# Performance work log

Measured on AMD Instinct MI355X. Metric: run time of the kernel, lower is better.

The kernel has to match this reference:

```python
import jax, jax.numpy as jnp
import numpy as np

DIM = 1536
NH = 12
HD = DIM // NH          # 128
C = HD // 2             # 64 complex freq slots per head
DT = C - 2 * (C // 3)   # 22 temporal
DS = C // 3             # 21 per spatial axis
EPS = 1e-6
M_TAB = 64              # rope table length (>= max(f,h,w))


def _rope_tables():
    def tab(d):
        inv = 1.0 / (10000.0 ** (np.arange(d, dtype=np.float64) / d))
        ang = np.outer(np.arange(M_TAB, dtype=np.float64), inv)
        return np.cos(ang), np.sin(ang)
    ct, st = tab(DT)
    ch, sh = tab(DS)
    cw, sw = tab(DS)
    fc = np.concatenate([ct, ch, cw], axis=1).astype(np.float32)  # [M, 64]
    fs = np.concatenate([st, sh, sw], axis=1).astype(np.float32)
    return jnp.asarray(fc), jnp.asarray(fs)


def setup_inputs() -> dict:
    key = jax.random.key(0)
    ks = jax.random.split(key, 6)
    B, F, H, W = 1, 8, 22, 40
    L = F * H * W  # 7040
    s = 0.02
    x = jax.random.normal(ks[0], (B, L, DIM), jnp.float32)
    Wq = jax.random.normal(ks[1], (DIM, DIM), jnp.float32) * s
    Wk = jax.random.normal(ks[2], (DIM, DIM), jnp.float32) * s
    Wv = jax.random.normal(ks[3], (DIM, DIM), jnp.float32) * s
    Wo = jax.random.normal(ks[4], (DIM, DIM), jnp.float32) * s
    bk2 = jax.random.split(ks[5], 4)
    bq = jax.random.normal(bk2[0], (DIM,), jnp.float32) * s
    bk = jax.random.normal(bk2[1], (DIM,), jnp.float32) * s
    bv = jax.random.normal(bk2[2], (DIM,), jnp.float32) * s
    bo = jax.random.normal(bk2[3], (DIM,), jnp.float32) * s
    fc, fs = _rope_tables()
    return dict(x=x, Wq=Wq, bq=bq, Wk=Wk, bk=bk, Wv=Wv, bv=bv, Wo=Wo, bo=bo,
                gq=jnp.ones((DIM,), jnp.float32), gk=jnp.ones((DIM,), jnp.float32),
                freqs_cos=fc, freqs_sin=fs,
                num_frames=F, grid_h=H, grid_w=W,
                chunk_size=2, sink_size=1, max_attention_size=2640)


def _pos_table(tab, f, h, w):
    # tab: [M, 64] -> per-token [f*h*w, 64] via (t,h,w) axis split [22,21,21]
    t = jnp.broadcast_to(tab[:f, :DT][:, None, None, :], (f, h, w, DT))
    hh = jnp.broadcast_to(tab[:h, DT:DT + DS][None, :, None, :], (f, h, w, DS))
    ww = jnp.broadcast_to(tab[:w, DT + DS:][None, None, :, :], (f, h, w, DS))
    return jnp.concatenate([t, hh, ww], axis=-1).reshape(f * h * w, C)


def _forward(x, Wq, bq, Wk, bk, Wv, bv, Wo, bo, gq, gk, freqs_cos, freqs_sin,
             num_frames, grid_h, grid_w, chunk_size, sink_size, max_attention_size):
    B, L, D = x.shape
    lin = lambda t, W, b: jnp.einsum('bld,ed->ble', t, W) + b
    rms = lambda t, g: t * jax.lax.rsqrt(jnp.mean(t * t, axis=-1, keepdims=True) + EPS) * g

    q = rms(lin(x, Wq, bq), gq).reshape(B, L, NH, HD)
    k = rms(lin(x, Wk, bk), gk).reshape(B, L, NH, HD)
    v = lin(x, Wv, bv).reshape(B, L, NH, HD)

    # causal RoPE (start_frame=0)
    cosL = _pos_table(freqs_cos, num_frames, grid_h, grid_w)  # [L, 64]
    sinL = _pos_table(freqs_sin, num_frames, grid_h, grid_w)

    def rope(t):
        a = t.reshape(B, L, NH, C, 2)
        xr, xi = a[..., 0], a[..., 1]
        co = cosL[None, :, None, :]
        si = sinL[None, :, None, :]
        return jnp.stack([xr * co - xi * si, xr * si + xi * co], axis=-1).reshape(B, L, NH, HD)

    q = rope(q)
    k = rope(k)

    # loop attention, diffusion forcing: chunk i attends [0,(i+1)*block) with sink+window
    frame_seqlen = grid_h * grid_w
    block = frame_seqlen * chunk_size
    total_len = num_frames * frame_seqlen
    sink_end = sink_size * frame_seqlen
    num_chunks = -(-total_len // block)
    scale = 1.0 / (HD ** 0.5)

    def attn(qi, ki, vi):
        s = jnp.einsum('bqnd,bknd->bnqk', qi, ki) * scale
        p = jax.nn.softmax(s, axis=-1)
        return jnp.einsum('bnqk,bknd->bqnd', p, vi)

    outs = []
    for i in range(num_chunks):
        q_start = i * block
        q_end = min((i + 1) * block, total_len)
        qi = q[:, q_start:q_end]
        chunk_end = q_end
        if max_attention_size == -1 or sink_end == 0:
            if max_attention_size == -1:
                ki, vi = k[:, :chunk_end], v[:, :chunk_end]
            else:
                ws = max(0, chunk_end - max_attention_size)
                ki, vi = k[:, ws:chunk_end], v[:, ws:chunk_end]
        else:
            window = max_attention_size - sink_end
            ws = max(sink_end, chunk_end - window)
            ki = jnp.concatenate([k[:, :sink_end], k[:, ws:chunk_end]], axis=1)
            vi = jnp.concatenate([v[:, :sink_end], v[:, ws:chunk_end]], axis=1)
        outs.append(attn(qi, ki, vi))

    o = jnp.concatenate(outs, axis=1).reshape(B, L, D)
    return jnp.einsum('bld,ed->ble', o, Wo) + bo


def reference(x, Wq, bq, Wk, bk, Wv, bv, Wo, bo, gq, gk, freqs_cos, freqs_sin,
              num_frames, grid_h, grid_w, chunk_size, sink_size, max_attention_size):
    return _forward(x, Wq, bq, Wk, bk, Wv, bv, Wo, bo, gq, gk, freqs_cos, freqs_sin,
                    num_frames, grid_h, grid_w, chunk_size, sink_size, max_attention_size)
```

## Files before the change

kernel.cpp:

```cpp
#include <hip/hip_runtime.h>
#include <math.h>

typedef __attribute__((ext_vector_type(8))) short short8;
typedef __attribute__((ext_vector_type(4))) float f32x4;
typedef __attribute__((ext_vector_type(16))) float f32x16;
typedef __attribute__((ext_vector_type(4))) float f4;
typedef __attribute__((ext_vector_type(4))) unsigned short us4;
typedef __attribute__((ext_vector_type(2))) unsigned int u32x2;

#define MFMA16(a,b,c) __builtin_amdgcn_mfma_f32_16x16x32_bf16(a,b,c,0,0,0)
#define MFMA32(a,b,c) __builtin_amdgcn_mfma_f32_32x32x16_bf16(a,b,c,0,0,0)

__device__ __forceinline__ unsigned short f2bf(float f) {
  unsigned int u = __float_as_uint(f);
  u = (u + 0x7FFFu + ((u >> 16) & 1u)) >> 16;
  return (unsigned short)u;
}
__device__ __forceinline__ float bf2f(unsigned short b) {
  return __uint_as_float(((unsigned int)b) << 16);
}
__device__ __forceinline__ unsigned int pk2(float a, float b) {
  unsigned int au = __float_as_uint(a) + 0x8000u;
  unsigned int bu = __float_as_uint(b) + 0x8000u;
  return __builtin_amdgcn_perm(bu, au, 0x07060302u);
}

typedef const __attribute__((address_space(1))) unsigned int* gas_t;
typedef __attribute__((address_space(3))) unsigned int* las_t;
__device__ __forceinline__ void gl16(const void* g, void* l) {
  __builtin_amdgcn_global_load_lds((gas_t)g, (las_t)l, 16, 0, 0);
}

__global__ void cvt_f32_bf16(const float* __restrict__ in,
                             unsigned short* __restrict__ out, int n4) {
  int i = blockIdx.x * blockDim.x + threadIdx.x;
  const int stride = gridDim.x * blockDim.x;
  for (; i < n4; i += stride) {
    f4 v = ((const f4*)in)[i];
    us4 o;
    o[0] = f2bf(v[0]); o[1] = f2bf(v[1]); o[2] = f2bf(v[2]); o[3] = f2bf(v[3]);
    ((us4*)out)[i] = o;
  }
}

__global__ void cvt4_f32_bf16(const float* __restrict__ w0, const float* __restrict__ w1,
                              const float* __restrict__ w2, const float* __restrict__ w3,
                              unsigned short* __restrict__ o0, unsigned short* __restrict__ o1,
                              unsigned short* __restrict__ o2, unsigned short* __restrict__ o3,
                              int n4) {
  const float* in = (blockIdx.y == 0) ? w0 : (blockIdx.y == 1) ? w1 : (blockIdx.y == 2) ? w2 : w3;
  unsigned short* out = (blockIdx.y == 0) ? o0 : (blockIdx.y == 1) ? o1 : (blockIdx.y == 2) ? o2 : o3;
  int i = blockIdx.x * blockDim.x + threadIdx.x;
  const int stride = gridDim.x * blockDim.x;
  for (; i < n4; i += stride) {
    f4 v = ((const f4*)in)[i];
    us4 o;
    o[0] = f2bf(v[0]); o[1] = f2bf(v[1]); o[2] = f2bf(v[2]); o[3] = f2bf(v[3]);
    ((us4*)out)[i] = o;
  }
}

template<int F32OUT>
__global__ __launch_bounds__(256)
void gemm_bt(const unsigned short* __restrict__ A,
             const unsigned short* __restrict__ B,
             const float* __restrict__ bias,
             unsigned short* __restrict__ obf,
             float* __restrict__ of32,
             int K, int ldo, int nbx, int q, int r)
{
  const int lin = blockIdx.x;
  const int xcd = lin & 7, local = lin >> 3;
  const int wg = (xcd < r) ? (xcd * (q + 1) + local) : (r * (q + 1) + (xcd - r) * q + local);
  const int m0 = (wg / nbx) * 128, n0 = (wg % nbx) * 128;

  const int tid = threadIdx.x;
  const int wave = tid >> 6, lane = tid & 63, lg = lane >> 4, lr = lane & 15;
  const int wr = wave >> 1, wc = wave & 1;

  __shared__ __align__(16) unsigned short Al[128 * 32];
  __shared__ __align__(16) unsigned short Bl[128 * 32];

  f32x4 acc[4][4];
#pragma unroll
  for (int m = 0; m < 4; ++m)
#pragma unroll
    for (int n = 0; n < 4; ++n) acc[m][n] = (f32x4){0.f, 0.f, 0.f, 0.f};

  const int r0 = tid >> 2, r1 = (tid + 256) >> 2;
  const int c0 = (tid & 3) * 8;
  const long arow0 = (long)(m0 + r0) * K, arow1 = (long)(m0 + r1) * K;
  const long brow0 = (long)(n0 + r0) * K, brow1 = (long)(n0 + r1) * K;

  for (int k0 = 0; k0 < K; k0 += 32) {
    gl16(A + arow0 + k0 + c0, (char*)Al + tid * 16);
    gl16(A + arow1 + k0 + c0, (char*)Al + (tid + 256) * 16);
    gl16(B + brow0 + k0 + c0, (char*)Bl + tid * 16);
    gl16(B + brow1 + k0 + c0, (char*)Bl + (tid + 256) * 16);
    __syncthreads();
    short8 af[4], bf[4];
#pragma unroll
    for (int m = 0; m < 4; ++m)
      af[m] = *(const short8*)(Al + (wr * 64 + m * 16 + lr) * 32 + lg * 8);
#pragma unroll
    for (int n = 0; n < 4; ++n)
      bf[n] = *(const short8*)(Bl + (wc * 64 + n * 16 + lr) * 32 + lg * 8);
#pragma unroll
    for (int m = 0; m < 4; ++m)
#pragma unroll
      for (int n = 0; n < 4; ++n)
        acc[m][n] = MFMA16(af[m], bf[n], acc[m][n]);
    __syncthreads();
  }

#pragma unroll
  for (int n = 0; n < 4; ++n) {
    const int col = n0 + wc * 64 + n * 16 + lr;
    const float bs = bias[col];
#pragma unroll
    for (int m = 0; m < 4; ++m) {
      const int row = m0 + wr * 64 + m * 16 + lg * 4;
#pragma unroll
      for (int r2 = 0; r2 < 4; ++r2) {
        float v = acc[m][n][r2] + bs;
        if (F32OUT) of32[(long)(row + r2) * ldo + col] = v;
        else        obf[(long)(row + r2) * ldo + col] = f2bf(v);
      }
    }
  }
}

__global__ __launch_bounds__(256)
void normrope(unsigned short* __restrict__ qkv, const float* __restrict__ gq,
              const float* __restrict__ gk,
              const float* __restrict__ fc, const float* __restrict__ fs,
              float qsc)
{
  const int l = blockIdx.x, tid = threadIdx.x;
  const int colOff = blockIdx.y ? 1536 : 0;
  const float* g = blockIdx.y ? gk : gq;
  const float oscale = blockIdx.y ? 1.0f : qsc;
  __shared__ float rowbuf[1536];
  __shared__ float sred[4];
  unsigned short* rp = qkv + (long)l * 4608 + colOff;

  float ss = 0.f;
  if (tid < 192) {
    short8 v = *(const short8*)(rp + tid * 8);
#pragma unroll
    for (int e = 0; e < 8; ++e) {
      float f = bf2f((unsigned short)v[e]);
      rowbuf[tid * 8 + e] = f;
      ss += f * f;
    }
  }
#pragma unroll
  for (int m = 32; m; m >>= 1) ss += __shfl_xor(ss, m, 64);
  if ((tid & 63) == 0) sred[tid >> 6] = ss;
  __syncthreads();
  const float rs = rsqrtf((sred[0] + sred[1] + sred[2] + sred[3]) * (1.f / 1536.f) + 1e-6f);

  const int f_ = l / 880, rem = l % 880, h_ = rem / 40, w_ = rem % 40;
#pragma unroll
  for (int j = 0; j < 3; ++j) {
    int p = tid + j * 256;
    int head = p >> 6, c = p & 63;
    int e = head * 128 + 2 * c;
    int tr = (c < 22) ? f_ : ((c < 43) ? h_ : w_);
    float co = fc[tr * 64 + c], si = fs[tr * 64 + c];
    float xr = rowbuf[e] * rs * g[e];
    float xi = rowbuf[e + 1] * rs * g[e + 1];
    float yr = (xr * co - xi * si) * oscale;
    float yi = (xr * si + xi * co) * oscale;
    unsigned int pk = (unsigned int)f2bf(yr) | ((unsigned int)f2bf(yi) << 16);
    *(unsigned int*)(rp + e) = pk;
  }
}

__device__ __forceinline__ void issueK(const unsigned short* __restrict__ qkv,
                                       int h, int t, int kvlen, int woff, int tid,
                                       unsigned short* Kbuf)
{
#pragma unroll
  for (int i = 0; i < 4; ++i) {
    int s = i * 256 + tid;
    int kvl = s >> 4;
    int dc = (s & 15) ^ (kvl & 7);
    int j = t * 64 + kvl; j = j < kvlen ? j : kvlen - 1;
    int gk = j + (j >= 880 ? woff : 0);
    gl16(qkv + (long)gk * 4608 + 1536 + h * 128 + dc * 8, (char*)Kbuf + s * 16);
  }
}

__device__ __forceinline__ void loadV(const unsigned short* __restrict__ qkv,
                                      int h, int t, int kvlen, int woff, int tid,
                                      short8 vp[2][2])
{
#pragma unroll
  for (int i = 0; i < 2; ++i) {
    int task = i * 256 + tid;
    int dc = task & 15, kp = task >> 4;
    int kvl = kp * 2;
    int j0 = t * 64 + kvl, j1 = j0 + 1;
    j0 = j0 < kvlen ? j0 : kvlen - 1;
    j1 = j1 < kvlen ? j1 : kvlen - 1;
    int g0 = j0 + (j0 >= 880 ? woff : 0);
    int g1 = j1 + (j1 >= 880 ? woff : 0);
    vp[i][0] = *(const short8*)(qkv + (long)g0 * 4608 + 3072 + h * 128 + dc * 8);
    vp[i][1] = *(const short8*)(qkv + (long)g1 * 4608 + 3072 + h * 128 + dc * 8);
  }
}

__device__ __forceinline__ void writeV(int tid, short8 vp[2][2], unsigned short* Vt)
{
#pragma unroll
  for (int i = 0; i < 2; ++i) {
    int task = i * 256 + tid;
    int dc = task & 15, kp = task >> 4;
    int kvl = kp * 2;
#pragma unroll
    for (int e = 0; e < 8; ++e) {
      int d = dc * 8 + e;
      int byte = d * 128 + kvl * 2;
      byte ^= (((d & 7) ^ ((d >> 3) & 7)) << 4);
      *(unsigned int*)((char*)Vt + byte) =
          (unsigned int)(unsigned short)vp[i][0][e] |
          ((unsigned int)(unsigned short)vp[i][1][e] << 16);
    }
  }
}

__global__ __launch_bounds__(256, 2)
void attn_kern(const unsigned short* __restrict__ qkv,
               unsigned short* __restrict__ ob)
{
  const int qt = blockIdx.x, ci = blockIdx.y, h = blockIdx.z;
  const int tid = threadIdx.x, wave = tid >> 6, lane = tid & 63;
  const int l31 = lane & 31, hh = lane >> 5;
  const int chunk_start = ci * 1760, chunk_end = chunk_start + 1760;
  const int wstart = (ci == 0) ? 880 : ci * 1760;
  const int woff = wstart - 880;
  const int kvlen = 880 + (chunk_end - wstart);
  const int q0 = chunk_start + qt * 128;

  __shared__ __align__(16) unsigned short Kl[2][64 * 128];
  __shared__ __align__(16) unsigned short Vt[2][128 * 64];

  int qr = q0 + wave * 32 + l31;
  if (qr >= chunk_end) qr = chunk_end - 1;
  const unsigned short* qp = qkv + (long)qr * 4608 + h * 128;
  short8 qf[8];
#pragma unroll
  for (int st = 0; st < 8; ++st) qf[st] = *(const short8*)(qp + st * 16 + hh * 8);

  f32x16 Oc[4];
#pragma unroll
  for (int i = 0; i < 4; ++i)
#pragma unroll
    for (int j = 0; j < 16; ++j) Oc[i][j] = 0.f;
  float m_run = -1e30f, l_run = 0.f;
  unsigned int w0[8], w1[8];

  auto computeQK = [&](int t, int cur, f32x16* S0, f32x16* S1) {
    f32x16 a0, a1;
#pragma unroll
    for (int j = 0; j < 16; ++j) { a0[j] = 0.f; a1[j] = 0.f; }
    __builtin_amdgcn_s_setprio(1);
#pragma unroll
    for (int st = 0; st < 8; ++st) {
      int off = 32 * st + 16 * hh;
      int b0 = l31 * 256 + (off ^ ((l31 & 7) << 4));
      short8 k0 = *(const short8*)((const char*)&Kl[cur][0] + b0);
      a0 = MFMA32(k0, qf[st], a0);
      int b1 = (32 + l31) * 256 + (off ^ ((l31 & 7) << 4));
      short8 k1 = *(const short8*)((const char*)&Kl[cur][0] + b1);
      a1 = MFMA32(k1, qf[st], a1);
    }
    __builtin_amdgcn_s_setprio(0);
    if (t * 64 + 64 > kvlen) {
#pragma unroll
      for (int r = 0; r < 16; ++r) {
        int kv0 = t * 64 + (r & 3) + 8 * (r >> 2) + 4 * hh;
        if (kv0 >= kvlen)      a0[r] = -1e30f;
        if (kv0 + 32 >= kvlen) a1[r] = -1e30f;
      }
    }
    *S0 = a0; *S1 = a1;
  };

  auto finishTile = [&](f32x16& s0f, f32x16& s1f) {
    float mx[16];
#pragma unroll
    for (int r = 0; r < 16; ++r) mx[r] = fmaxf(s0f[r], s1f[r]);
#pragma unroll
    for (int w = 8; w; w >>= 1)
#pragma unroll
      for (int r = 0; r < w; ++r) mx[r] = fmaxf(mx[r], mx[r + w]);
    float pm = fmaxf(mx[0], __shfl_xor(mx[0], 32, 64));
    const bool defer = __all(pm <= m_run + 8.f);
    const float mn = defer ? m_run : fmaxf(m_run, pm);
#pragma unroll
    for (int r = 0; r < 16; ++r) {
      s0f[r] = __builtin_amdgcn_exp2f(s0f[r] - mn);
      s1f[r] = __builtin_amdgcn_exp2f(s1f[r] - mn);
    }
    float sm[16];
#pragma unroll
    for (int r = 0; r < 16; ++r) sm[r] = s0f[r] + s1f[r];
#pragma unroll
    for (int w = 8; w; w >>= 1)
#pragma unroll
      for (int r = 0; r < w; ++r) sm[r] += sm[r + w];
    float sum = sm[0] + __shfl_xor(sm[0], 32, 64);
    if (defer) {
      l_run += sum;
    } else {
      float al = __builtin_amdgcn_exp2f(m_run - mn);
      l_run = l_run * al + sum;
      m_run = mn;
#pragma unroll
      for (int i = 0; i < 4; ++i)
#pragma unroll
        for (int j = 0; j < 16; ++j) Oc[i][j] *= al;
    }
#pragma unroll
    for (int m = 0; m < 8; ++m) {
      w0[m] = pk2(s0f[2 * m], s0f[2 * m + 1]);
      w1[m] = pk2(s1f[2 * m], s1f[2 * m + 1]);
    }
  };

  auto doPV = [&](int cur) {
    __builtin_amdgcn_s_setprio(1);
#pragma unroll
    for (int s = 0; s < 4; ++s) {
      const unsigned int* w = (s < 2) ? w0 : w1;
      const int lo4 = (s & 1) * 4;
      unsigned int x0 = __shfl_xor(w[lo4 + 2], 32, 64);
      unsigned int x1 = __shfl_xor(w[lo4 + 3], 32, 64);
      unsigned int y0 = __shfl_xor(w[lo4],     32, 64);
      unsigned int y1 = __shfl_xor(w[lo4 + 1], 32, 64);
      unsigned int fw[4];
      fw[0] = hh ? x0 : w[lo4];
      fw[1] = hh ? x1 : w[lo4 + 1];
      fw[2] = hh ? w[lo4 + 2] : y0;
      fw[3] = hh ? w[lo4 + 3] : y1;
      short8 pb = *(const short8*)fw;
#pragma unroll
      for (int dt = 0; dt < 4; ++dt) {
        int d = dt * 32 + l31;
        int byte = d * 128 + s * 32 + hh * 16;
        byte ^= (((d & 7) ^ ((d >> 3) & 7)) << 4);
        short8 vf = *(const short8*)((const char*)&Vt[cur][0] + byte);
        Oc[dt] = MFMA32(vf, pb, Oc[dt]);
      }
    }
    __builtin_amdgcn_s_setprio(0);
  };

  const int nt = (kvlen + 63) >> 6;
  short8 vp[2][2];

  issueK(qkv, h, 0, kvlen, woff, tid, &Kl[0][0]);
  if (nt > 1) issueK(qkv, h, 1, kvlen, woff, tid, &Kl[1][0]);
  loadV(qkv, h, 0, kvlen, woff, tid, vp);
  writeV(tid, vp, &Vt[0][0]);
  __syncthreads();

  f32x16 sp0, sp1;
  computeQK(0, 0, &sp0, &sp1);
  __syncthreads();

  for (int t = 0; t < nt - 1; ++t) {
    const int cur = t & 1;
    if (t + 2 < nt) issueK(qkv, h, t + 2, kvlen, woff, tid, &Kl[cur][0]);
    loadV(qkv, h, t + 1, kvlen, woff, tid, vp);

    f32x16 sc0, sc1;
    computeQK(t + 1, cur ^ 1, &sc0, &sc1);
    finishTile(sp0, sp1);
    writeV(tid, vp, &Vt[cur ^ 1][0]);
    doPV(cur);
    __syncthreads();
    sp0 = sc0; sp1 = sc1;
  }
  finishTile(sp0, sp1);
  doPV((nt - 1) & 1);

  const int qg = q0 + wave * 32 + l31;
  if (qg < chunk_end) {
    const float inv = 1.f / l_run;
    unsigned short* op = ob + (long)qg * 1536 + h * 128;
#pragma unroll
    for (int dt = 0; dt < 4; ++dt) {
#pragma unroll
      for (int gblk = 0; gblk < 4; ++gblk) {
        int d = dt * 32 + gblk * 8 + hh * 4;
        unsigned int u0 = pk2(Oc[dt][4 * gblk]     * inv, Oc[dt][4 * gblk + 1] * inv);
        unsigned int u1 = pk2(Oc[dt][4 * gblk + 2] * inv, Oc[dt][4 * gblk + 3] * inv);
        u32x2 uu; uu[0] = u0; uu[1] = u1;
        *(u32x2*)(op + d) = uu;
      }
    }
  }
}

extern "C" void kernel_launch(void* const* d_in, const int* in_sizes, int n_in,
                              void* d_out, int out_size, void* d_ws, size_t ws_size,
                              hipStream_t stream)
{
  const float* x  = (const float*)d_in[0];
  const float* Wq = (const float*)d_in[1];
  const float* bq = (const float*)d_in[2];
  const float* Wk = (const float*)d_in[3];
  const float* bk = (const float*)d_in[4];
  const float* Wv = (const float*)d_in[5];
  const float* bv = (const float*)d_in[6];
  const float* Wo = (const float*)d_in[7];
  const float* bo = (const float*)d_in[8];
  const float* gq = (const float*)d_in[9];
  const float* gk = (const float*)d_in[10];
  const float* fc = (const float*)d_in[11];
  const float* fs = (const float*)d_in[12];

  char* ws = (char*)d_ws;
  unsigned short* xb   = (unsigned short*)(ws);
  unsigned short* wcat = (unsigned short*)(ws + 21626880);
  unsigned short* wob  = (unsigned short*)(ws + 35782656);
  float*          bcat = (float*)(ws + 40501248);
  unsigned short* qkv  = (unsigned short*)(ws + 40519680);
  unsigned short* obuf = (unsigned short*)(ws + 105400320);

  cvt_f32_bf16<<<2048, 256, 0, stream>>>(x, xb, 10813440 / 4);
  cvt4_f32_bf16<<<dim3(576, 4), 256, 0, stream>>>(
      Wq, Wk, Wv, Wo,
      wcat, wcat + 2359296, wcat + 4718592, wob, 2359296 / 4);
  hipMemcpyAsync(bcat,        bq, 1536 * 4, hipMemcpyDeviceToDevice, stream);
  hipMemcpyAsync(bcat + 1536, bk, 1536 * 4, hipMemcpyDeviceToDevice, stream);
  hipMemcpyAsync(bcat + 3072, bv, 1536 * 4, hipMemcpyDeviceToDevice, stream);

  gemm_bt<0><<<1980, 256, 0, stream>>>(xb, wcat, bcat, qkv, nullptr, 1536, 4608,
                                       36, 1980 / 8, 1980 % 8);

  const float qsc = (float)(1.4426950408889634 / sqrt(128.0));
  normrope<<<dim3(7040, 2), 256, 0, stream>>>(qkv, gq, gk, fc, fs, qsc);

  attn_kern<<<dim3(14, 4, 12), 256, 0, stream>>>(qkv, obuf);

  gemm_bt<1><<<660, 256, 0, stream>>>(obuf, wob, bo, nullptr, (float*)d_out, 1536, 1536,
                                      12, 660 / 8, 660 % 8);
}
```

Measured before the change: 439.1 us.

## Replace QKV projection GEMM with 256x256 double-buffered pipelined MFMA kernel

The QKV projection moves to a new 512-thread kernel that computes 256x256 tiles with a 64-wide K step. It double-buffers LDS with an XOR swizzle, prefetches A one step and B two steps ahead, and interleaves loads with MFMA phases using barriers and s_setprio. This targets global-load latency and low data reuse in the old 128x128 kernel. The M dimension is padded to 7168 rows, so the workspace is relaid out with obuf aliased onto the x bf16 buffer to hold the extra A rows the kernel reads. That aliasing risks reading or overwriting stale data.

```diff
diff --git a/kernel.cpp b/kernel.cpp
--- a/kernel.cpp
+++ b/kernel.cpp
@@ -60,12 +60,119 @@
   }
 }
 
-template<int F32OUT>
+__global__ __launch_bounds__(512, 1)
+void gemm8(const unsigned short* __restrict__ A,
+           const unsigned short* __restrict__ B,
+           const float* __restrict__ bias,
+           unsigned short* __restrict__ out)
+{
+  const int bi = blockIdx.x;
+  const int wg = (bi & 7) * 63 + (bi >> 3);
+  const int m0 = (wg / 18) * 256, n0 = (wg % 18) * 256;
+
+  const int tid = threadIdx.x;
+  const int lane = tid & 63, lg = lane >> 4, lr = lane & 15;
+  const int wave = tid >> 6, wr = wave >> 2, wc = wave & 3;
+
+  __shared__ __align__(16) unsigned short Ab[2][256 * 64];
+  __shared__ __align__(16) unsigned short Bb[2][256 * 64];
+
+  f32x4 acc[8][4];
+#pragma unroll
+  for (int m = 0; m < 8; ++m)
+#pragma unroll
+    for (int n = 0; n < 4; ++n) acc[m][n] = (f32x4){0.f, 0.f, 0.f, 0.f};
+
+  auto stage = [&](const unsigned short* P, int rowBase, int t, unsigned short* lbase) {
+    const int k0 = t * 64;
+#pragma unroll
+    for (int i = 0; i < 2; ++i) {
+      int s = i * 512 + tid;
+      int row = s >> 3, c = s & 7;
+      int cc = c ^ (row & 7);
+      gl16(P + (long)(rowBase + row) * 1536 + k0 + cc * 8, (char*)lbase + s * 16);
+    }
+  };
+  auto rdA = [&](int buf, int mr, int k) -> short8 {
+    int row = mr + lr;
+    int byte = (row * 128 + (k + lg * 8) * 2) ^ ((row & 7) << 4);
+    return *(const short8*)((const char*)&Ab[buf][0] + byte);
+  };
+  auto rdB = [&](int buf, int nr, int k) -> short8 {
+    int row = nr + lr;
+    int byte = (row * 128 + (k + lg * 8) * 2) ^ ((row & 7) << 4);
+    return *(const short8*)((const char*)&Bb[buf][0] + byte);
+  };
+
+  stage(A, m0,       0, &Ab[0][0]);
+  stage(A, m0 + 128, 0, &Ab[0][128 * 64]);
+  stage(B, n0,       0, &Bb[0][0]);
+  stage(B, n0 + 128, 0, &Bb[0][128 * 64]);
+  stage(B, n0,       1, &Bb[1][0]);
+  stage(B, n0 + 128, 1, &Bb[1][128 * 64]);
+  asm volatile("s_waitcnt vmcnt(4)" ::: "memory");
+  __builtin_amdgcn_s_barrier();
+
+  for (int T = 0; T < 24; ++T) {
+    const int cur = T & 1;
+    const int tA = (T + 1 < 24) ? T + 1 : 23;
+    const int tB = (T + 2 < 24) ? T + 2 : 23;
+    short8 bfr[4][2];
+#pragma unroll
+    for (int p = 0; p < 4; ++p) {
+      if (p == 0)      stage(A, m0,       tA, &Ab[cur ^ 1][0]);
+      else if (p == 1) stage(A, m0 + 128, tA, &Ab[cur ^ 1][128 * 64]);
+      else if (p == 2) stage(B, n0,       tB, &Bb[cur][0]);
+      else             stage(B, n0 + 128, tB, &Bb[cur][128 * 64]);
+      if (p == 0) {
+#pragma unroll
+        for (int n = 0; n < 4; ++n) {
+          bfr[n][0] = rdB(cur, wc * 64 + n * 16, 0);
+          bfr[n][1] = rdB(cur, wc * 64 + n * 16, 32);
+        }
+      }
+      short8 afr[2][2];
+#pragma unroll
+      for (int m2 = 0; m2 < 2; ++m2) {
+        afr[m2][0] = rdA(cur, wr * 128 + p * 32 + m2 * 16, 0);
+        afr[m2][1] = rdA(cur, wr * 128 + p * 32 + m2 * 16, 32);
+      }
+      if (p == 3) asm volatile("s_waitcnt vmcnt(4)" ::: "memory");
+      __builtin_amdgcn_s_barrier();
+      __builtin_amdgcn_s_setprio(1);
+#pragma unroll
+      for (int m2 = 0; m2 < 2; ++m2)
+#pragma unroll
+        for (int n = 0; n < 4; ++n) {
+          acc[p * 2 + m2][n] = MFMA16(afr[m2][0], bfr[n][0], acc[p * 2 + m2][n]);
+          acc[p * 2 + m2][n] = MFMA16(afr[m2][1], bfr[n][1], acc[p * 2 + m2][n]);
+        }
+      __builtin_amdgcn_s_setprio(0);
+      __builtin_amdgcn_s_barrier();
+    }
+  }
+  asm volatile("s_waitcnt vmcnt(0)" ::: "memory");
+
+#pragma unroll
+  for (int n = 0; n < 4; ++n) {
+    const int col = n0 + wc * 64 + n * 16 + lr;
+    const float bs = bias[col];
+#pragma unroll
+    for (int m = 0; m < 8; ++m) {
+      const int row = m0 + wr * 128 + m * 16 + lg * 4;
+#pragma unroll
+      for (int r = 0; r < 4; ++r) {
+        if (row + r < 7040)
+          out[(long)(row + r) * 4608 + col] = f2bf(acc[m][n][r] + bs);
+      }
+    }
+  }
+}
+
 __global__ __launch_bounds__(256)
 void gemm_bt(const unsigned short* __restrict__ A,
              const unsigned short* __restrict__ B,
              const float* __restrict__ bias,
-             unsigned short* __restrict__ obf,
              float* __restrict__ of32,
              int K, int ldo, int nbx, int q, int r)
 {
@@ -121,11 +228,8 @@
     for (int m = 0; m < 4; ++m) {
       const int row = m0 + wr * 64 + m * 16 + lg * 4;
 #pragma unroll
-      for (int r2 = 0; r2 < 4; ++r2) {
-        float v = acc[m][n][r2] + bs;
-        if (F32OUT) of32[(long)(row + r2) * ldo + col] = v;
-        else        obf[(long)(row + r2) * ldo + col] = f2bf(v);
-      }
+      for (int r2 = 0; r2 < 4; ++r2)
+        of32[(long)(row + r2) * ldo + col] = acc[m][n][r2] + bs;
     }
   }
 }
@@ -425,11 +529,11 @@
 
   char* ws = (char*)d_ws;
   unsigned short* xb   = (unsigned short*)(ws);
-  unsigned short* wcat = (unsigned short*)(ws + 21626880);
-  unsigned short* wob  = (unsigned short*)(ws + 35782656);
-  float*          bcat = (float*)(ws + 40501248);
-  unsigned short* qkv  = (unsigned short*)(ws + 40519680);
-  unsigned short* obuf = (unsigned short*)(ws + 105400320);
+  unsigned short* obuf = xb;
+  unsigned short* wcat = (unsigned short*)(ws + 22020096);
+  unsigned short* wob  = (unsigned short*)(ws + 36175872);
+  float*          bcat = (float*)(ws + 40894464);
+  unsigned short* qkv  = (unsigned short*)(ws + 40912896);
 
   cvt_f32_bf16<<<2048, 256, 0, stream>>>(x, xb, 10813440 / 4);
   cvt4_f32_bf16<<<dim3(576, 4), 256, 0, stream>>>(
@@ -439,14 +543,13 @@
   hipMemcpyAsync(bcat + 1536, bk, 1536 * 4, hipMemcpyDeviceToDevice, stream);
   hipMemcpyAsync(bcat + 3072, bv, 1536 * 4, hipMemcpyDeviceToDevice, stream);
 
-  gemm_bt<0><<<1980, 256, 0, stream>>>(xb, wcat, bcat, qkv, nullptr, 1536, 4608,
-                                       36, 1980 / 8, 1980 % 8);
+  gemm8<<<504, 512, 0, stream>>>(xb, wcat, bcat, qkv);
 
   const float qsc = (float)(1.4426950408889634 / sqrt(128.0));
   normrope<<<dim3(7040, 2), 256, 0, stream>>>(qkv, gq, gk, fc, fs, qsc);
 
   attn_kern<<<dim3(14, 4, 12), 256, 0, stream>>>(qkv, obuf);
 
-  gemm_bt<1><<<660, 256, 0, stream>>>(obuf, wob, bo, nullptr, (float*)d_out, 1536, 1536,
-                                      12, 660 / 8, 660 % 8);
-}
+  gemm_bt<<<660, 256, 0, stream>>>(obuf, wob, bo, (float*)d_out, 1536, 1536,
+                                   12, 660 / 8, 660 % 8);
+}
```

Result: no change. 434.0 us (-1.2%).
